# Optimization experiments

Hardware: AMD Instinct MI355X
Metric: run time of the kernel (lower is better)

## Reference

```python
import jax, jax.numpy as jnp
import numpy as np

LOG_2PI = float(np.log(2.0 * np.pi))
EPS = 1e-10


def setup_inputs() -> dict:
    key = jax.random.key(0)
    k1, k2, k3, k4, k5 = jax.random.split(key, 5)
    N, B, C, V = 32768, 32, 32, 16
    x = jax.random.normal(k1, (N, 6), dtype=jnp.float32)
    vote_6d = jax.random.normal(k2, (B, C, V, 6), dtype=jnp.float32)
    scales = jax.random.uniform(k3, (B, C, V), dtype=jnp.float32)
    log_pres = jax.random.normal(k4, (B, C, V), dtype=jnp.float32)
    batch = jnp.sort(jax.random.randint(k5, (N,), 0, B, dtype=jnp.int64))
    return {"x": x, "vote_6d": vote_6d, "scales": scales, "log_pres": log_pres, "batch": batch}


def reference(x, vote_6d, scales, log_pres, batch):
    # x: [N, 6]; vote_6d: [B, C, V, 6]; scales/log_pres: [B, C, V]; batch: [N]
    B = vote_6d.shape[0]
    safe_scale = jnp.clip(scales, EPS)                 # clamp(scale, min=eps)
    mu = vote_6d[batch]                                # [N, C, V, 6] gather by batch idx
    s = safe_scale[batch][..., None]                   # [N, C, V, 1] broadcast over 6 dims
    prior = log_pres[batch]                            # [N, C, V]
    xe = x[:, None, None, :]                           # [N, 1, 1, 6]
    z = (xe - mu) / s
    # Normal log-prob per dim, summed over the 6 pose dims
    vote_log_prob = jnp.sum(-0.5 * z * z - jnp.log(s) - 0.5 * LOG_2PI, axis=-1)  # [N, C, V]
    posterior_logits = prior + vote_log_prob           # [N, C, V]
    N = posterior_logits.shape[0]
    log_prob_per_point = jax.nn.logsumexp(posterior_logits.reshape(N, -1), axis=-1)  # [N]
    log_prob_per_example = jax.ops.segment_sum(log_prob_per_point, batch, num_segments=B)  # [B]
    log_prob_batch = jnp.mean(log_prob_per_example)
    return log_prob_batch, log_prob_per_example
```

## Files before the change

### kernel.cpp

```cpp
#include <hip/hip_runtime.h>
#include <math.h>

#define LOG_2PI_F 1.8378770664093453f
#define EPS_F 1e-10f
#define NB 32
#define CV 512
#define PPW 8
#define KPL 8

__global__ __launch_bounds__(256)
__attribute__((amdgpu_waves_per_eu(2, 4)))
void capsule_main(
    const float* __restrict__ x,
    const float* __restrict__ vote,
    const float* __restrict__ scales,
    const float* __restrict__ log_pres,
    const int* __restrict__ batch,
    float* __restrict__ out_pe,
    float* __restrict__ wsum,
    int n_pts)
{
    const int tid  = threadIdx.x;
    const int lane = tid & 63;
    const int wave = blockIdx.x * (blockDim.x >> 6) + (tid >> 6);
    const int p0   = wave * PPW;
    if (p0 >= n_pts) return;

    int pidx = p0 + (lane & 7);
    if (pidx >= n_pts) pidx = n_pts - 1;
    const int  pb8     = batch[pidx];
    const int  b0      = __builtin_amdgcn_readfirstlane(pb8);
    const bool uniform = (__ballot(pb8 == b0) == ~0ull);

    float a0[KPL], a1[KPL], a2[KPL], a3[KPL], a4[KPL], a5[KPL];
    float ainv[KPL], acoef[KPL];

    auto load_params = [&](int b) {
        #pragma unroll
        for (int j = 0; j < KPL; ++j) {
            const int c = b * CV + lane + 64 * j;
            float s   = fmaxf(scales[c], EPS_F);
            float inv = 1.0f / s;
            const float* mu = vote + (size_t)c * 6;
            a0[j] = mu[0] * inv;
            a1[j] = mu[1] * inv;
            a2[j] = mu[2] * inv;
            a3[j] = mu[3] * inv;
            a4[j] = mu[4] * inv;
            a5[j] = mu[5] * inv;
            ainv[j]  = inv;
            acoef[j] = log_pres[c] - 6.0f * __logf(s) - 3.0f * LOG_2PI_F;
        }
    };

    load_params(b0);

    auto point_lse = [&](int p) -> float {
        const float* xp = x + (size_t)p * 6;
        const float x0 = xp[0], x1 = xp[1], x2 = xp[2],
                    x3 = xp[3], x4 = xp[4], x5 = xp[5];
        float l[KPL];
        #pragma unroll
        for (int j = 0; j < KPL; ++j) {
            float z, acc;
            z = fmaf(x0, ainv[j], -a0[j]); acc = z * z;
            z = fmaf(x1, ainv[j], -a1[j]); acc = fmaf(z, z, acc);
            z = fmaf(x2, ainv[j], -a2[j]); acc = fmaf(z, z, acc);
            z = fmaf(x3, ainv[j], -a3[j]); acc = fmaf(z, z, acc);
            z = fmaf(x4, ainv[j], -a4[j]); acc = fmaf(z, z, acc);
            z = fmaf(x5, ainv[j], -a5[j]); acc = fmaf(z, z, acc);
            l[j] = fmaf(acc, -0.5f, acoef[j]);
        }
        float lm = fmaxf(fmaxf(fmaxf(l[0], l[1]), fmaxf(l[2], l[3])),
                         fmaxf(fmaxf(l[4], l[5]), fmaxf(l[6], l[7])));
        #pragma unroll
        for (int off = 1; off <= 32; off <<= 1)
            lm = fmaxf(lm, __shfl_xor(lm, off, 64));
        float e0 = __expf(l[0] - lm) + __expf(l[1] - lm);
        float e1 = __expf(l[2] - lm) + __expf(l[3] - lm);
        float e2 = __expf(l[4] - lm) + __expf(l[5] - lm);
        float e3 = __expf(l[6] - lm) + __expf(l[7] - lm);
        float es = (e0 + e1) + (e2 + e3);
        #pragma unroll
        for (int off = 1; off <= 32; off <<= 1)
            es += __shfl_xor(es, off, 64);
        return lm + __logf(es);
    };

    if (uniform && p0 + PPW <= n_pts) {
        float wavesum = 0.0f;
        #pragma unroll
        for (int q = 0; q < PPW; ++q)
            wavesum += point_lse(p0 + q);
        if (lane == 0) wsum[wave] = wavesum;
    } else {
        if (lane == 0) wsum[wave] = 0.0f;
        int cur_b = b0;
        for (int q = 0; q < PPW; ++q) {
            const int p = p0 + q;
            if (p >= n_pts) break;
            const int pb = batch[p];
            if (pb != cur_b) { load_params(pb); cur_b = pb; }
            float lp = point_lse(p);
            if (lane == 0) atomicAdd(&out_pe[cur_b], lp);
        }
    }
}

__global__ __launch_bounds__(1024) void final_kernel(
    const float* __restrict__ wsum,
    const int* __restrict__ batch,
    float* __restrict__ d_out,
    int n_waves, int n_pts)
{
    __shared__ float part[NB];
    const int t = threadIdx.x;
    if (t < NB) part[t] = 0.0f;
    __syncthreads();

    for (int w = t; w < n_waves; w += 1024) {
        float s = wsum[w];
        int   pi = w * PPW;
        if (pi >= n_pts) pi = n_pts - 1;
        atomicAdd(&part[batch[pi]], s);
    }
    __syncthreads();

    if (t < 64) {
        float v = 0.0f;
        if (t < NB) {
            v = d_out[1 + t] + part[t];
            d_out[1 + t] = v;
        }
        #pragma unroll
        for (int off = 32; off >= 1; off >>= 1) v += __shfl_xor(v, off, 64);
        if (t == 0) d_out[0] = v * (1.0f / NB);
    }
}

extern "C" void kernel_launch(void* const* d_in, const int* in_sizes, int n_in,
                              void* d_out, int out_size, void* d_ws, size_t ws_size,
                              hipStream_t stream) {
    const float* x        = (const float*)d_in[0];
    const float* vote     = (const float*)d_in[1];
    const float* scales   = (const float*)d_in[2];
    const float* log_pres = (const float*)d_in[3];
    const int*   batch    = (const int*)d_in[4];
    float* out = (float*)d_out;
    float* ws  = (float*)d_ws;

    int n_pts   = in_sizes[0] / 6;
    int n_waves = (n_pts + PPW - 1) / PPW;

    hipMemsetAsync(d_out, 0, (size_t)out_size * sizeof(float), stream);

    int n_blocks = (n_waves + 3) / 4;
    capsule_main<<<n_blocks, 256, 0, stream>>>(x, vote, scales, log_pres, batch,
                                               out + 1, ws, n_pts);

    final_kernel<<<1, 1024, 0, stream>>>(ws, batch, out, n_waves, n_pts);
}
```

Before: 93.03 us.

## Fuse final reduction into main kernel via last-block counter

Merges the separate single-block reduction kernel into the main kernel. Each block bumps an atomic counter, and the last block to finish sums the per-wave partials and boundary atomics into the outputs. The memset now zeroes a small workspace region instead of the output. It also prefetches the next point's coordinates inside the uniform path to overlap loads with compute. This removes one kernel launch and its gap, at the cost of a block-wide sync, a threadfence per block, and a serial tail done by 256 threads instead of 1024.

```diff
diff --git a/kernel.cpp b/kernel.cpp
--- a/kernel.cpp
+++ b/kernel.cpp
@@ -10,131 +10,148 @@
 
 __global__ __launch_bounds__(256)
 __attribute__((amdgpu_waves_per_eu(2, 4)))
-void capsule_main(
+void capsule_fused(
     const float* __restrict__ x,
     const float* __restrict__ vote,
     const float* __restrict__ scales,
     const float* __restrict__ log_pres,
     const int* __restrict__ batch,
-    float* __restrict__ out_pe,
-    float* __restrict__ wsum,
-    int n_pts)
+    float* __restrict__ out,
+    float* __restrict__ ws,
+    int n_pts, int n_waves)
 {
+    __shared__ float part[NB];
+    __shared__ unsigned int is_last;
+
     const int tid  = threadIdx.x;
     const int lane = tid & 63;
-    const int wave = blockIdx.x * (blockDim.x >> 6) + (tid >> 6);
+    const int wloc = __builtin_amdgcn_readfirstlane(tid >> 6);
+    const int wave = blockIdx.x * 4 + wloc;
     const int p0   = wave * PPW;
-    if (p0 >= n_pts) return;
 
-    int pidx = p0 + (lane & 7);
-    if (pidx >= n_pts) pidx = n_pts - 1;
-    const int  pb8     = batch[pidx];
-    const int  b0      = __builtin_amdgcn_readfirstlane(pb8);
-    const bool uniform = (__ballot(pb8 == b0) == ~0ull);
+    unsigned int* ctr  = (unsigned int*)ws;
+    float*        bnd  = ws + 1;
+    float*        wsum = ws + 64;
 
-    float a0[KPL], a1[KPL], a2[KPL], a3[KPL], a4[KPL], a5[KPL];
-    float ainv[KPL], acoef[KPL];
+    if (p0 < n_pts) {
+        int pidx = p0 + (lane & 7);
+        if (pidx >= n_pts) pidx = n_pts - 1;
+        const int  pb8     = batch[pidx];
+        const int  b0      = __builtin_amdgcn_readfirstlane(pb8);
+        const bool uniform = (__ballot(pb8 == b0) == ~0ull);
 
-    auto load_params = [&](int b) {
-        #pragma unroll
-        for (int j = 0; j < KPL; ++j) {
-            const int c = b * CV + lane + 64 * j;
-            float s   = fmaxf(scales[c], EPS_F);
-            float inv = 1.0f / s;
-            const float* mu = vote + (size_t)c * 6;
-            a0[j] = mu[0] * inv;
-            a1[j] = mu[1] * inv;
-            a2[j] = mu[2] * inv;
-            a3[j] = mu[3] * inv;
-            a4[j] = mu[4] * inv;
-            a5[j] = mu[5] * inv;
-            ainv[j]  = inv;
-            acoef[j] = log_pres[c] - 6.0f * __logf(s) - 3.0f * LOG_2PI_F;
-        }
-    };
+        float a0[KPL], a1[KPL], a2[KPL], a3[KPL], a4[KPL], a5[KPL];
+        float ainv[KPL], acoef[KPL];
 
-    load_params(b0);
+        auto load_params = [&](int b) {
+            #pragma unroll
+            for (int j = 0; j < KPL; ++j) {
+                const int c = b * CV + lane + 64 * j;
+                float s   = fmaxf(scales[c], EPS_F);
+                float inv = 1.0f / s;
+                const float* mu = vote + (size_t)c * 6;
+                a0[j] = mu[0] * inv;
+                a1[j] = mu[1] * inv;
+                a2[j] = mu[2] * inv;
+                a3[j] = mu[3] * inv;
+                a4[j] = mu[4] * inv;
+                a5[j] = mu[5] * inv;
+                ainv[j]  = inv;
+                acoef[j] = log_pres[c] - 6.0f * __logf(s) - 3.0f * LOG_2PI_F;
+            }
+        };
 
-    auto point_lse = [&](int p) -> float {
-        const float* xp = x + (size_t)p * 6;
-        const float x0 = xp[0], x1 = xp[1], x2 = xp[2],
-                    x3 = xp[3], x4 = xp[4], x5 = xp[5];
-        float l[KPL];
-        #pragma unroll
-        for (int j = 0; j < KPL; ++j) {
-            float z, acc;
-            z = fmaf(x0, ainv[j], -a0[j]); acc = z * z;
-            z = fmaf(x1, ainv[j], -a1[j]); acc = fmaf(z, z, acc);
-            z = fmaf(x2, ainv[j], -a2[j]); acc = fmaf(z, z, acc);
-            z = fmaf(x3, ainv[j], -a3[j]); acc = fmaf(z, z, acc);
-            z = fmaf(x4, ainv[j], -a4[j]); acc = fmaf(z, z, acc);
-            z = fmaf(x5, ainv[j], -a5[j]); acc = fmaf(z, z, acc);
-            l[j] = fmaf(acc, -0.5f, acoef[j]);
-        }
-        float lm = fmaxf(fmaxf(fmaxf(l[0], l[1]), fmaxf(l[2], l[3])),
-                         fmaxf(fmaxf(l[4], l[5]), fmaxf(l[6], l[7])));
-        #pragma unroll
-        for (int off = 1; off <= 32; off <<= 1)
-            lm = fmaxf(lm, __shfl_xor(lm, off, 64));
-        float e0 = __expf(l[0] - lm) + __expf(l[1] - lm);
-        float e1 = __expf(l[2] - lm) + __expf(l[3] - lm);
-        float e2 = __expf(l[4] - lm) + __expf(l[5] - lm);
-        float e3 = __expf(l[6] - lm) + __expf(l[7] - lm);
-        float es = (e0 + e1) + (e2 + e3);
-        #pragma unroll
-        for (int off = 1; off <= 32; off <<= 1)
-            es += __shfl_xor(es, off, 64);
-        return lm + __logf(es);
-    };
+        load_params(b0);
 
-    if (uniform && p0 + PPW <= n_pts) {
-        float wavesum = 0.0f;
-        #pragma unroll
-        for (int q = 0; q < PPW; ++q)
-            wavesum += point_lse(p0 + q);
-        if (lane == 0) wsum[wave] = wavesum;
-    } else {
-        if (lane == 0) wsum[wave] = 0.0f;
-        int cur_b = b0;
-        for (int q = 0; q < PPW; ++q) {
-            const int p = p0 + q;
-            if (p >= n_pts) break;
-            const int pb = batch[p];
-            if (pb != cur_b) { load_params(pb); cur_b = pb; }
-            float lp = point_lse(p);
-            if (lane == 0) atomicAdd(&out_pe[cur_b], lp);
+        auto lse = [&](float x0, float x1, float x2,
+                       float x3, float x4, float x5) -> float {
+            float l[KPL];
+            #pragma unroll
+            for (int j = 0; j < KPL; ++j) {
+                float z, acc;
+                z = fmaf(x0, ainv[j], -a0[j]); acc = z * z;
+                z = fmaf(x1, ainv[j], -a1[j]); acc = fmaf(z, z, acc);
+                z = fmaf(x2, ainv[j], -a2[j]); acc = fmaf(z, z, acc);
+                z = fmaf(x3, ainv[j], -a3[j]); acc = fmaf(z, z, acc);
+                z = fmaf(x4, ainv[j], -a4[j]); acc = fmaf(z, z, acc);
+                z = fmaf(x5, ainv[j], -a5[j]); acc = fmaf(z, z, acc);
+                l[j] = fmaf(acc, -0.5f, acoef[j]);
+            }
+            float lm = fmaxf(fmaxf(fmaxf(l[0], l[1]), fmaxf(l[2], l[3])),
+                             fmaxf(fmaxf(l[4], l[5]), fmaxf(l[6], l[7])));
+            #pragma unroll
+            for (int off = 1; off <= 32; off <<= 1)
+                lm = fmaxf(lm, __shfl_xor(lm, off, 64));
+            float e0 = __expf(l[0] - lm) + __expf(l[1] - lm);
+            float e1 = __expf(l[2] - lm) + __expf(l[3] - lm);
+            float e2 = __expf(l[4] - lm) + __expf(l[5] - lm);
+            float e3 = __expf(l[6] - lm) + __expf(l[7] - lm);
+            float es = (e0 + e1) + (e2 + e3);
+            #pragma unroll
+            for (int off = 1; off <= 32; off <<= 1)
+                es += __shfl_xor(es, off, 64);
+            return lm + __logf(es);
+        };
+
+        if (uniform && p0 + PPW <= n_pts) {
+            const float* xp = x + (size_t)p0 * 6;
+            float cx0 = xp[0], cx1 = xp[1], cx2 = xp[2],
+                  cx3 = xp[3], cx4 = xp[4], cx5 = xp[5];
+            float wavesum = 0.0f;
+            #pragma unroll
+            for (int q = 0; q < PPW; ++q) {
+                const float x0 = cx0, x1 = cx1, x2 = cx2,
+                            x3 = cx3, x4 = cx4, x5 = cx5;
+                if (q + 1 < PPW) {
+                    const float* xn = x + (size_t)(p0 + q + 1) * 6;
+                    cx0 = xn[0]; cx1 = xn[1]; cx2 = xn[2];
+                    cx3 = xn[3]; cx4 = xn[4]; cx5 = xn[5];
+                }
+                wavesum += lse(x0, x1, x2, x3, x4, x5);
+            }
+            if (lane == 0) wsum[wave] = wavesum;
+        } else {
+            if (lane == 0) wsum[wave] = 0.0f;
+            int cur_b = b0;
+            for (int q = 0; q < PPW; ++q) {
+                const int p = p0 + q;
+                if (p >= n_pts) break;
+                const int pb = batch[p];
+                if (pb != cur_b) { load_params(pb); cur_b = pb; }
+                const float* xp = x + (size_t)p * 6;
+                float lp = lse(xp[0], xp[1], xp[2], xp[3], xp[4], xp[5]);
+                if (lane == 0) atomicAdd(&bnd[cur_b], lp);
+            }
         }
     }
-}
 
-__global__ __launch_bounds__(1024) void final_kernel(
-    const float* __restrict__ wsum,
-    const int* __restrict__ batch,
-    float* __restrict__ d_out,
-    int n_waves, int n_pts)
-{
-    __shared__ float part[NB];
-    const int t = threadIdx.x;
-    if (t < NB) part[t] = 0.0f;
     __syncthreads();
-
-    for (int w = t; w < n_waves; w += 1024) {
-        float s = wsum[w];
-        int   pi = w * PPW;
-        if (pi >= n_pts) pi = n_pts - 1;
-        atomicAdd(&part[batch[pi]], s);
+    if (tid == 0) {
+        __threadfence();
+        unsigned int done = atomicAdd(ctr, 1u);
+        is_last = (done == gridDim.x - 1u) ? 1u : 0u;
     }
     __syncthreads();
 
-    if (t < 64) {
-        float v = 0.0f;
-        if (t < NB) {
-            v = d_out[1 + t] + part[t];
-            d_out[1 + t] = v;
+    if (is_last) {
+        __threadfence();
+        if (tid < NB) part[tid] = bnd[tid];
+        __syncthreads();
+        for (int w = tid; w < n_waves; w += 256) {
+            float s = wsum[w];
+            int pi = w * PPW;
+            if (pi >= n_pts) pi = n_pts - 1;
+            atomicAdd(&part[batch[pi]], s);
         }
-        #pragma unroll
-        for (int off = 32; off >= 1; off >>= 1) v += __shfl_xor(v, off, 64);
-        if (t == 0) d_out[0] = v * (1.0f / NB);
+        __syncthreads();
+        if (tid < 64) {
+            float v = (tid < NB) ? part[tid] : 0.0f;
+            if (tid < NB) out[1 + tid] = v;
+            #pragma unroll
+            for (int off = 32; off >= 1; off >>= 1)
+                v += __shfl_xor(v, off, 64);
+            if (tid == 0) out[0] = v * (1.0f / NB);
+        }
     }
 }
 
@@ -152,11 +169,9 @@
     int n_pts   = in_sizes[0] / 6;
     int n_waves = (n_pts + PPW - 1) / PPW;
 
-    hipMemsetAsync(d_out, 0, (size_t)out_size * sizeof(float), stream);
+    hipMemsetAsync(d_ws, 0, 256, stream);
 
     int n_blocks = (n_waves + 3) / 4;
-    capsule_main<<<n_blocks, 256, 0, stream>>>(x, vote, scales, log_pres, batch,
-                                               out + 1, ws, n_pts);
-
-    final_kernel<<<1, 1024, 0, stream>>>(ws, batch, out, n_waves, n_pts);
+    capsule_fused<<<n_blocks, 256, 0, stream>>>(x, vote, scales, log_pres,
+                                                batch, out, ws, n_pts, n_waves);
 }
```

New measurement: 103.2 us. +10.9%, slower.
